# Kernel tuning notes

Measured on AMD Instinct MI355X. Metric: run time of the kernel, lower is better.

The kernel has to match this reference:

```python
import jax, jax.numpy as jnp
import numpy as np
from jax.scipy.special import logsumexp

N, C, D = 400000, 256, 3


def setup_inputs() -> dict:
    key = jax.random.key(0)
    k1, k2 = jax.random.split(key)
    X = jax.random.normal(k1, (N, D), dtype=jnp.float32)
    mu = jax.random.normal(k2, (C, D), dtype=jnp.float32)
    w = jnp.zeros((C,), dtype=jnp.float32)
    # sigma as in __init__: 0.1 * (r / C**(1/D)), r = sqrt(sum of per-dim variances of mu)
    r = jnp.sqrt(jnp.var(mu, axis=0).sum())
    sigma = (0.1 * (r / C ** (1.0 / D)))[None].astype(jnp.float32)
    return {"X": X, "mu": mu, "w": w, "sigma": sigma}


def reference(X, mu, w, sigma):
    """One EM step of the uniform-covariance GMM (no outliers). Returns (Y, Cfe)."""
    n, d = X.shape
    sig = sigma[0]
    # E-step: squared distances (N,C) and log-responsibilities
    D2_nc = jnp.sum((X[:, None, :] - mu[None, :, :]) ** 2, axis=-1)  # (N,C)
    loggaussnorm = d * (jnp.log(sig) + 0.5 * jnp.log(2.0 * jnp.pi))
    Zw = logsumexp(w)
    t_nc = w[None, :] - Zw - D2_nc / (2.0 * sig ** 2) - loggaussnorm  # (N,C)
    T_n = logsumexp(t_nc, axis=1)
    lgamma_nc = t_nc - T_n[:, None]
    gamma_nc = jnp.exp(lgamma_nc)
    # M-step updates (order matters, as in the torch code)
    mu_new = jax.nn.softmax(lgamma_nc, axis=0).T @ X            # (C,D)
    w_new = logsumexp(lgamma_nc, axis=0)                        # (C,)
    sig_new = jnp.sqrt(jnp.sum(gamma_nc * D2_nc) / (d * n))     # scalar
    # Quadratic targets Y_n = sum_c gamma_nc * mu_c (with updated mu)
    Y = gamma_nc @ mu_new                                       # (N,D)
    # Free-energy offset (loggaussnorm uses OLD sigma; 1/(2 sigma^2) uses NEW sigma)
    lpi_c = w_new - logsumexp(w_new)
    Cfe = jnp.sum(
        gamma_nc
        * (
            (jnp.sum(mu_new ** 2, axis=-1)[None, :] - jnp.sum(Y ** 2, axis=-1)[:, None])
            / (2.0 * sig_new ** 2)
            + loggaussnorm
            + lgamma_nc
            - lpi_c[None, :]
        )
    )
    return Y, Cfe
```

## Files before the change

kernel.cpp:

```cpp
#include <hip/hip_runtime.h>
#include <math.h>

#define CC   256
#define TILE 256

#define OFF_P     0
#define OFF_Q     1024
#define OFF_S     2048
#define OFF_CD    3072
#define OFF_CF    3080
#define OFF_T2    3088

__device__ __forceinline__ float fexp2(float x) { return __builtin_amdgcn_exp2f(x); }
__device__ __forceinline__ float flog2(float x) { return __builtin_amdgcn_logf(x); }

__global__ __launch_bounds__(256) void gmm_prep(const float* __restrict__ mu,
                                                const float* __restrict__ w,
                                                const float* __restrict__ sigma,
                                                float* __restrict__ ws)
{
    __shared__ float redA[4], redB[4];
    const int c = threadIdx.x;
    const int lane = c & 63, wid = c >> 6;

    ws[OFF_S + c] = 0.f; ws[OFF_S + 256 + c] = 0.f;
    ws[OFF_S + 512 + c] = 0.f; ws[OFF_S + 768 + c] = 0.f;
    if (c < 4) ((double*)(ws + OFF_CD))[c] = 0.0;
    if (c >= 8 && c < 16) ws[OFF_CF + (c - 6)] = 0.f;

    float wc = w[c];
    float m = wc;
    #pragma unroll
    for (int off = 32; off > 0; off >>= 1) m = fmaxf(m, __shfl_xor(m, off));
    if (lane == 0) redA[wid] = m;
    __syncthreads();
    m = fmaxf(fmaxf(redA[0], redA[1]), fmaxf(redA[2], redA[3]));
    float e = expf(wc - m);
    #pragma unroll
    for (int off = 32; off > 0; off >>= 1) e += __shfl_xor(e, off);
    if (lane == 0) redB[wid] = e;
    __syncthreads();
    float Zw = m + logf(redB[0] + redB[1] + redB[2] + redB[3]);

    const float L = 1.4426950408889634f;
    float sig = sigma[0];
    float lgn = 3.0f * (logf(sig) + 0.91893853320467274f);
    float k = L / (2.0f * sig * sig);
    float twok = 2.0f * k;
    float mx = mu[3*c], my = mu[3*c+1], mz = mu[3*c+2];
    float m2 = mx*mx + my*my + mz*mz;
    float alpha = (wc - Zw - lgn) * L - k * m2;
    ((float4*)(ws + OFF_P))[c] = make_float4(twok*mx, twok*my, twok*mz, alpha);
    if (c == 0) { ws[OFF_CF + 0] = twok; ws[OFF_CF + 1] = lgn; }
}

__global__ __launch_bounds__(256) void gmm_pass1(const float* __restrict__ X,
                                                 float* __restrict__ ws, int N)
{
    __shared__ float4 Psh[CC];
    __shared__ float4 XT[TILE];
    __shared__ float2 msP[2][TILE];
    __shared__ float4 Bpart[CC];
    __shared__ double redd[2][4];

    const int tid  = threadIdx.x;
    const int pi   = tid & 127;
    const int half = tid >> 7;
    const int n0   = blockIdx.x * TILE;
    const int NT   = min(TILE, N - n0);

    Psh[tid] = ((const float4*)(ws + OFF_P))[tid];

    const int i0 = pi, i1 = pi + 128;
    const bool v0 = i0 < NT, v1 = i1 < NT;
    float x0=0.f,y0=0.f,z0=0.f, x1=0.f,y1=0.f,z1=0.f;
    if (v0) { const float* p = X + 3*(size_t)(n0+i0); x0=p[0]; y0=p[1]; z0=p[2]; }
    if (v1) { const float* p = X + 3*(size_t)(n0+i1); x1=p[0]; y1=p[1]; z1=p[2]; }
    float q0 = fmaf(x0,x0, fmaf(y0,y0, z0*z0));
    float q1 = fmaf(x1,x1, fmaf(y1,y1, z1*z1));
    __syncthreads();

    const float4* Pc = Psh + half*128;
    float m0=-3.0e38f, m1=-3.0e38f, s0=0.f, s1=0.f;
    #pragma unroll 8
    for (int c = 0; c < 128; ++c) {
        float4 p = Pc[c];
        float u0 = fmaf(x0,p.x, fmaf(y0,p.y, fmaf(z0,p.z, p.w)));
        float u1 = fmaf(x1,p.x, fmaf(y1,p.y, fmaf(z1,p.z, p.w)));
        float a0 = fmaxf(m0,u0), a1 = fmaxf(m1,u1);
        if (__any((u0>m0) || (u1>m1))) {
            s0 *= fexp2(m0-a0); s1 *= fexp2(m1-a1);
            m0 = a0; m1 = a1;
        }
        s0 += fexp2(u0-m0);
        s1 += fexp2(u1-m1);
    }
    msP[half][i0] = make_float2(m0, s0);
    msP[half][i1] = make_float2(m1, s1);
    __syncthreads();

    double xd = 0.0, td = 0.0;
    if (half == 0) {
        if (v0) {
            float2 a = msP[0][i0], b = msP[1][i0];
            float M = fmaxf(a.x, b.x);
            float T2 = M + flog2(a.y*fexp2(a.x-M) + b.y*fexp2(b.x-M));
            XT[i0] = make_float4(x0,y0,z0,T2);
            ws[OFF_T2 + n0 + i0] = T2;
            xd += (double)q0; td += (double)T2;
        }
        if (v1) {
            float2 a = msP[0][i1], b = msP[1][i1];
            float M = fmaxf(a.x, b.x);
            float T2 = M + flog2(a.y*fexp2(a.x-M) + b.y*fexp2(b.x-M));
            XT[i1] = make_float4(x1,y1,z1,T2);
            ws[OFF_T2 + n0 + i1] = T2;
            xd += (double)q1; td += (double)T2;
        }
    }
    {
        const int lane = tid & 63, wid = tid >> 6;
        #pragma unroll
        for (int off = 32; off > 0; off >>= 1) { xd += __shfl_xor(xd, off); td += __shfl_xor(td, off); }
        if (lane == 0) { redd[0][wid] = xd; redd[1][wid] = td; }
    }
    __syncthreads();
    if (tid == 0) {
        double* CD = (double*)(ws + OFF_CD);
        atomicAdd(CD + 0, redd[0][0]+redd[0][1]+redd[0][2]+redd[0][3]);
        atomicAdd(CD + 1, redd[1][0]+redd[1][1]+redd[1][2]+redd[1][3]);
    }

    float4 pA = Psh[pi], pB = Psh[pi + 128];
    float SA=0.f,AxA=0.f,AyA=0.f,AzA=0.f, SB=0.f,AxB=0.f,AyB=0.f,AzB=0.f;
    const int nlo = half*128, nhi = min(nlo+128, NT);
    #pragma unroll 8
    for (int n = nlo; n < nhi; ++n) {
        float4 xt = XT[n];
        float uA = fmaf(xt.x,pA.x, fmaf(xt.y,pA.y, fmaf(xt.z,pA.z, pA.w)));
        float uB = fmaf(xt.x,pB.x, fmaf(xt.y,pB.y, fmaf(xt.z,pB.z, pB.w)));
        float gA = fexp2(uA - xt.w);
        float gB = fexp2(uB - xt.w);
        SA+=gA; AxA=fmaf(gA,xt.x,AxA); AyA=fmaf(gA,xt.y,AyA); AzA=fmaf(gA,xt.z,AzA);
        SB+=gB; AxB=fmaf(gB,xt.x,AxB); AyB=fmaf(gB,xt.y,AyB); AzB=fmaf(gB,xt.z,AzB);
    }
    if (half == 1) {
        Bpart[pi]       = make_float4(SA,AxA,AyA,AzA);
        Bpart[pi + 128] = make_float4(SB,AxB,AyB,AzB);
    }
    __syncthreads();
    if (half == 0) {
        float4 bA = Bpart[pi], bB = Bpart[pi + 128];
        SA+=bA.x; AxA+=bA.y; AyA+=bA.z; AzA+=bA.w;
        SB+=bB.x; AxB+=bB.y; AyB+=bB.z; AzB+=bB.w;
        float* Sg = ws + OFF_S;
        atomicAdd(Sg       + pi, SA);   atomicAdd(Sg       + pi + 128, SB);
        atomicAdd(Sg + 256 + pi, AxA);  atomicAdd(Sg + 256 + pi + 128, AxB);
        atomicAdd(Sg + 512 + pi, AyA);  atomicAdd(Sg + 512 + pi + 128, AyB);
        atomicAdd(Sg + 768 + pi, AzA);  atomicAdd(Sg + 768 + pi + 128, AzB);
    }
}

__global__ __launch_bounds__(256) void gmm_pass2(float* __restrict__ ws, int N)
{
    __shared__ double red6[6][4];
    const int c = threadIdx.x;
    const int lane = c & 63, wid = c >> 6;
    const float twok = ws[OFF_CF + 0];
    const double invt = 1.0 / (double)twok;
    double* CD = (double*)(ws + OFF_CD);

    float Sc  = ws[OFF_S       + c];
    float Axc = ws[OFF_S + 256 + c];
    float Ayc = ws[OFF_S + 512 + c];
    float Azc = ws[OFF_S + 768 + c];
    float4 p  = ((const float4*)(ws + OFF_P))[c];

    float inv = 1.0f / fmaxf(Sc, 1e-37f);
    float mx = Axc * inv, my = Ayc * inv, mz = Azc * inv;
    ((float4*)(ws + OFF_Q))[c] = make_float4(mx, my, mz, 0.f);

    double v0 = (double)Sc;
    double v1 = (double)Sc * (double)(mx*mx + my*my + mz*mz);
    double v2 = (double)Sc * log((double)fmaxf(Sc, 1e-37f));
    double v3 = (double)Sc * (double)(p.x*p.x + p.y*p.y + p.z*p.z);
    double v4 = (double)Sc * (double)p.w;
    double v5 = (double)(p.x*Axc + p.y*Ayc + p.z*Azc);

    #pragma unroll
    for (int off = 32; off > 0; off >>= 1) {
        v0 += __shfl_xor(v0, off); v1 += __shfl_xor(v1, off); v2 += __shfl_xor(v2, off);
        v3 += __shfl_xor(v3, off); v4 += __shfl_xor(v4, off); v5 += __shfl_xor(v5, off);
    }
    if (lane == 0) { red6[0][wid]=v0; red6[1][wid]=v1; red6[2][wid]=v2;
                     red6[3][wid]=v3; red6[4][wid]=v4; red6[5][wid]=v5; }
    __syncthreads();
    if (c == 0) {
        double sumS   = red6[0][0]+red6[0][1]+red6[0][2]+red6[0][3];
        double sumSM2 = red6[1][0]+red6[1][1]+red6[1][2]+red6[1][3];
        double sumSlS = red6[2][0]+red6[2][1]+red6[2][2]+red6[2][3];
        double sumMSs = red6[3][0]+red6[3][1]+red6[3][2]+red6[3][3];
        double sumAS  = red6[4][0]+red6[4][1]+red6[4][2]+red6[4][3];
        double dotMAs = red6[5][0]+red6[5][1]+red6[5][2]+red6[5][3];
        double sumX2  = CD[0];
        double sumT2  = CD[1];
        double sumGD2 = sumX2 + sumMSs*invt*invt - 2.0 * dotMAs*invt;
        double sn2    = sumGD2 / (3.0 * (double)N);
        ws[OFF_CF + 2] = (float)(1.0 / (2.0 * sn2));
        ws[OFF_CF + 3] = (float)(sumSlS - sumS * log(sumS));
        ws[OFF_CF + 4] = (float)(sumAS + dotMAs - sumT2);
        CD[3] = sumSM2;
    }
}

__global__ __launch_bounds__(256) void gmm_pass3(const float* __restrict__ X,
                                                 float* __restrict__ ws,
                                                 float* __restrict__ out, int N)
{
    __shared__ float4 Psh[CC], Qsh[CC];
    __shared__ float4 Yp[2][TILE];
    __shared__ double redd[4];

    const int tid  = threadIdx.x;
    const int pi   = tid & 127;
    const int half = tid >> 7;
    const int n0   = blockIdx.x * TILE;
    const int NT   = min(TILE, N - n0);

    Psh[tid] = ((const float4*)(ws + OFF_P))[tid];
    Qsh[tid] = ((const float4*)(ws + OFF_Q))[tid];

    const int i0 = pi, i1 = pi + 128;
    const bool v0 = i0 < NT, v1 = i1 < NT;
    float x0=0.f,y0=0.f,z0=0.f,T0=0.f, x1=0.f,y1=0.f,z1=0.f,T1=0.f;
    if (v0) { const float* p = X + 3*(size_t)(n0+i0); x0=p[0]; y0=p[1]; z0=p[2]; T0 = ws[OFF_T2+n0+i0]; }
    if (v1) { const float* p = X + 3*(size_t)(n0+i1); x1=p[0]; y1=p[1]; z1=p[2]; T1 = ws[OFF_T2+n0+i1]; }
    __syncthreads();

    const float4* Pc = Psh + half*128;
    const float4* Qc = Qsh + half*128;
    float Yx0=0.f,Yy0=0.f,Yz0=0.f, Yx1=0.f,Yy1=0.f,Yz1=0.f;
    #pragma unroll 8
    for (int c = 0; c < 128; ++c) {
        float4 p = Pc[c];
        float u0 = fmaf(x0,p.x, fmaf(y0,p.y, fmaf(z0,p.z, p.w)));
        float u1 = fmaf(x1,p.x, fmaf(y1,p.y, fmaf(z1,p.z, p.w)));
        float g0 = fexp2(u0 - T0);
        float g1 = fexp2(u1 - T1);
        float4 q = Qc[c];
        Yx0 = fmaf(g0,q.x,Yx0); Yy0 = fmaf(g0,q.y,Yy0); Yz0 = fmaf(g0,q.z,Yz0);
        Yx1 = fmaf(g1,q.x,Yx1); Yy1 = fmaf(g1,q.y,Yy1); Yz1 = fmaf(g1,q.z,Yz1);
    }
    Yp[half][i0] = make_float4(Yx0,Yy0,Yz0,0.f);
    Yp[half][i1] = make_float4(Yx1,Yy1,Yz1,0.f);
    __syncthreads();

    double y2d = 0.0;
    if (half == 0) {
        if (v0) {
            float4 a = Yp[0][i0], b = Yp[1][i0];
            float yx = a.x+b.x, yy = a.y+b.y, yz = a.z+b.z;
            float* op = out + 3*(size_t)(n0+i0);
            op[0]=yx; op[1]=yy; op[2]=yz;
            y2d += (double)yx*yx + (double)yy*yy + (double)yz*yz;
        }
        if (v1) {
            float4 a = Yp[0][i1], b = Yp[1][i1];
            float yx = a.x+b.x, yy = a.y+b.y, yz = a.z+b.z;
            float* op = out + 3*(size_t)(n0+i1);
            op[0]=yx; op[1]=yy; op[2]=yz;
            y2d += (double)yx*yx + (double)yy*yy + (double)yz*yz;
        }
    }
    {
        const int lane = tid & 63, wid = tid >> 6;
        #pragma unroll
        for (int off = 32; off > 0; off >>= 1) y2d += __shfl_xor(y2d, off);
        if (lane == 0) redd[wid] = y2d;
    }
    __syncthreads();
    if (tid == 0) atomicAdd(((double*)(ws + OFF_CD)) + 2, redd[0]+redd[1]+redd[2]+redd[3]);
}

__global__ void gmm_pass4(float* __restrict__ ws, float* __restrict__ cfe_out, int N)
{
    if (threadIdx.x == 0) {
        double* CD = (double*)(ws + OFF_CD);
        double Cfe = (CD[3] - CD[2]) * (double)ws[OFF_CF + 2]
                   + (double)N * (double)ws[OFF_CF + 1]
                   + 0.69314718055994531 * (double)ws[OFF_CF + 4]
                   - (double)ws[OFF_CF + 3];
        cfe_out[0] = (float)Cfe;
    }
}

extern "C" void kernel_launch(void* const* d_in, const int* in_sizes, int n_in,
                              void* d_out, int out_size, void* d_ws, size_t ws_size,
                              hipStream_t stream)
{
    const float* X     = (const float*)d_in[0];
    const float* mu    = (const float*)d_in[1];
    const float* w     = (const float*)d_in[2];
    const float* sigma = (const float*)d_in[3];
    float* out = (float*)d_out;
    float* ws  = (float*)d_ws;
    const int N = in_sizes[0] / 3;
    const int nblk = (N + TILE - 1) / TILE;

    gmm_prep <<<1,    256, 0, stream>>>(mu, w, sigma, ws);
    gmm_pass1<<<nblk, 256, 0, stream>>>(X, ws, N);
    gmm_pass2<<<1,    256, 0, stream>>>(ws, N);
    gmm_pass3<<<nblk, 256, 0, stream>>>(X, ws, out, N);
    gmm_pass4<<<1,    64,  0, stream>>>(ws, out + (size_t)3 * N, N);
}
```

Baseline: 112.6 us.

## Halve point tile to one point per thread and batch online-max rescaling

Shrinks the tile from 256 to 128 points so each thread handles one point instead of two in pass1 and pass3, doubling the grid and setting occupancy hints in launch bounds. The pass1 online logsumexp now computes 8 logits, takes their max, and does one wave-uniform rescale check per group instead of per component. This aims to raise occupancy and cut divergent branch overhead. The cost is that P/Q loads into shared memory and the atomics are amortized over fewer points, and the per-point work per loaded P entry is halved.

```diff
diff --git a/kernel.cpp b/kernel.cpp
--- a/kernel.cpp
+++ b/kernel.cpp
@@ -2,7 +2,7 @@
 #include <math.h>
 
 #define CC   256
-#define TILE 256
+#define TILE 128
 
 #define OFF_P     0
 #define OFF_Q     1024
@@ -54,8 +54,8 @@
     if (c == 0) { ws[OFF_CF + 0] = twok; ws[OFF_CF + 1] = lgn; }
 }
 
-__global__ __launch_bounds__(256) void gmm_pass1(const float* __restrict__ X,
-                                                 float* __restrict__ ws, int N)
+__global__ __launch_bounds__(256, 4) void gmm_pass1(const float* __restrict__ X,
+                                                    float* __restrict__ ws, int N)
 {
     __shared__ float4 Psh[CC];
     __shared__ float4 XT[TILE];
@@ -71,52 +71,43 @@
 
     Psh[tid] = ((const float4*)(ws + OFF_P))[tid];
 
-    const int i0 = pi, i1 = pi + 128;
-    const bool v0 = i0 < NT, v1 = i1 < NT;
-    float x0=0.f,y0=0.f,z0=0.f, x1=0.f,y1=0.f,z1=0.f;
-    if (v0) { const float* p = X + 3*(size_t)(n0+i0); x0=p[0]; y0=p[1]; z0=p[2]; }
-    if (v1) { const float* p = X + 3*(size_t)(n0+i1); x1=p[0]; y1=p[1]; z1=p[2]; }
+    const bool v0 = pi < NT;
+    float x0=0.f, y0=0.f, z0=0.f;
+    if (v0) { const float* p = X + 3*(size_t)(n0+pi); x0=p[0]; y0=p[1]; z0=p[2]; }
     float q0 = fmaf(x0,x0, fmaf(y0,y0, z0*z0));
-    float q1 = fmaf(x1,x1, fmaf(y1,y1, z1*z1));
     __syncthreads();
 
     const float4* Pc = Psh + half*128;
-    float m0=-3.0e38f, m1=-3.0e38f, s0=0.f, s1=0.f;
-    #pragma unroll 8
-    for (int c = 0; c < 128; ++c) {
-        float4 p = Pc[c];
-        float u0 = fmaf(x0,p.x, fmaf(y0,p.y, fmaf(z0,p.z, p.w)));
-        float u1 = fmaf(x1,p.x, fmaf(y1,p.y, fmaf(z1,p.z, p.w)));
-        float a0 = fmaxf(m0,u0), a1 = fmaxf(m1,u1);
-        if (__any((u0>m0) || (u1>m1))) {
-            s0 *= fexp2(m0-a0); s1 *= fexp2(m1-a1);
-            m0 = a0; m1 = a1;
+    float m0 = -3.0e38f, s0 = 0.f;
+    for (int c0 = 0; c0 < 128; c0 += 8) {
+        float u0[8];
+        #pragma unroll
+        for (int j = 0; j < 8; ++j) {
+            float4 p = Pc[c0 + j];
+            u0[j] = fmaf(x0,p.x, fmaf(y0,p.y, fmaf(z0,p.z, p.w)));
         }
-        s0 += fexp2(u0-m0);
-        s1 += fexp2(u1-m1);
-    }
-    msP[half][i0] = make_float2(m0, s0);
-    msP[half][i1] = make_float2(m1, s1);
+        float a = fmaxf(fmaxf(u0[0],u0[1]), fmaxf(u0[2],u0[3]));
+        float b = fmaxf(fmaxf(u0[4],u0[5]), fmaxf(u0[6],u0[7]));
+        float M = fmaxf(a, b);
+        if (__any(M > m0)) {
+            M = fmaxf(M, m0);
+            s0 *= fexp2(m0 - M);
+            m0 = M;
+        }
+        #pragma unroll
+        for (int j = 0; j < 8; ++j) s0 += fexp2(u0[j] - m0);
+    }
+    msP[half][pi] = make_float2(m0, s0);
     __syncthreads();
 
     double xd = 0.0, td = 0.0;
-    if (half == 0) {
-        if (v0) {
-            float2 a = msP[0][i0], b = msP[1][i0];
-            float M = fmaxf(a.x, b.x);
-            float T2 = M + flog2(a.y*fexp2(a.x-M) + b.y*fexp2(b.x-M));
-            XT[i0] = make_float4(x0,y0,z0,T2);
-            ws[OFF_T2 + n0 + i0] = T2;
-            xd += (double)q0; td += (double)T2;
-        }
-        if (v1) {
-            float2 a = msP[0][i1], b = msP[1][i1];
-            float M = fmaxf(a.x, b.x);
-            float T2 = M + flog2(a.y*fexp2(a.x-M) + b.y*fexp2(b.x-M));
-            XT[i1] = make_float4(x1,y1,z1,T2);
-            ws[OFF_T2 + n0 + i1] = T2;
-            xd += (double)q1; td += (double)T2;
-        }
+    if (half == 0 && v0) {
+        float2 a = msP[0][pi], b = msP[1][pi];
+        float M = fmaxf(a.x, b.x);
+        float T2 = M + flog2(a.y*fexp2(a.x-M) + b.y*fexp2(b.x-M));
+        XT[pi] = make_float4(x0,y0,z0,T2);
+        ws[OFF_T2 + n0 + pi] = T2;
+        xd = (double)q0; td = (double)T2;
     }
     {
         const int lane = tid & 63, wid = tid >> 6;
@@ -133,7 +124,7 @@
 
     float4 pA = Psh[pi], pB = Psh[pi + 128];
     float SA=0.f,AxA=0.f,AyA=0.f,AzA=0.f, SB=0.f,AxB=0.f,AyB=0.f,AzB=0.f;
-    const int nlo = half*128, nhi = min(nlo+128, NT);
+    const int nlo = half*64, nhi = min(nlo + 64, NT);
     #pragma unroll 8
     for (int n = nlo; n < nhi; ++n) {
         float4 xt = XT[n];
@@ -213,9 +204,9 @@
     }
 }
 
-__global__ __launch_bounds__(256) void gmm_pass3(const float* __restrict__ X,
-                                                 float* __restrict__ ws,
-                                                 float* __restrict__ out, int N)
+__global__ __launch_bounds__(256, 4) void gmm_pass3(const float* __restrict__ X,
+                                                    float* __restrict__ ws,
+                                                    float* __restrict__ out, int N)
 {
     __shared__ float4 Psh[CC], Qsh[CC];
     __shared__ float4 Yp[2][TILE];
@@ -230,47 +221,32 @@
     Psh[tid] = ((const float4*)(ws + OFF_P))[tid];
     Qsh[tid] = ((const float4*)(ws + OFF_Q))[tid];
 
-    const int i0 = pi, i1 = pi + 128;
-    const bool v0 = i0 < NT, v1 = i1 < NT;
-    float x0=0.f,y0=0.f,z0=0.f,T0=0.f, x1=0.f,y1=0.f,z1=0.f,T1=0.f;
-    if (v0) { const float* p = X + 3*(size_t)(n0+i0); x0=p[0]; y0=p[1]; z0=p[2]; T0 = ws[OFF_T2+n0+i0]; }
-    if (v1) { const float* p = X + 3*(size_t)(n0+i1); x1=p[0]; y1=p[1]; z1=p[2]; T1 = ws[OFF_T2+n0+i1]; }
+    const bool v0 = pi < NT;
+    float x0=0.f,y0=0.f,z0=0.f,T0=0.f;
+    if (v0) { const float* p = X + 3*(size_t)(n0+pi); x0=p[0]; y0=p[1]; z0=p[2]; T0 = ws[OFF_T2+n0+pi]; }
     __syncthreads();
 
     const float4* Pc = Psh + half*128;
     const float4* Qc = Qsh + half*128;
-    float Yx0=0.f,Yy0=0.f,Yz0=0.f, Yx1=0.f,Yy1=0.f,Yz1=0.f;
+    float Yx=0.f, Yy=0.f, Yz=0.f;
     #pragma unroll 8
     for (int c = 0; c < 128; ++c) {
         float4 p = Pc[c];
-        float u0 = fmaf(x0,p.x, fmaf(y0,p.y, fmaf(z0,p.z, p.w)));
-        float u1 = fmaf(x1,p.x, fmaf(y1,p.y, fmaf(z1,p.z, p.w)));
-        float g0 = fexp2(u0 - T0);
-        float g1 = fexp2(u1 - T1);
+        float u = fmaf(x0,p.x, fmaf(y0,p.y, fmaf(z0,p.z, p.w)));
+        float g = fexp2(u - T0);
         float4 q = Qc[c];
-        Yx0 = fmaf(g0,q.x,Yx0); Yy0 = fmaf(g0,q.y,Yy0); Yz0 = fmaf(g0,q.z,Yz0);
-        Yx1 = fmaf(g1,q.x,Yx1); Yy1 = fmaf(g1,q.y,Yy1); Yz1 = fmaf(g1,q.z,Yz1);
-    }
-    Yp[half][i0] = make_float4(Yx0,Yy0,Yz0,0.f);
-    Yp[half][i1] = make_float4(Yx1,Yy1,Yz1,0.f);
+        Yx = fmaf(g,q.x,Yx); Yy = fmaf(g,q.y,Yy); Yz = fmaf(g,q.z,Yz);
+    }
+    Yp[half][pi] = make_float4(Yx, Yy, Yz, 0.f);
     __syncthreads();
 
     double y2d = 0.0;
-    if (half == 0) {
-        if (v0) {
-            float4 a = Yp[0][i0], b = Yp[1][i0];
-            float yx = a.x+b.x, yy = a.y+b.y, yz = a.z+b.z;
-            float* op = out + 3*(size_t)(n0+i0);
-            op[0]=yx; op[1]=yy; op[2]=yz;
-            y2d += (double)yx*yx + (double)yy*yy + (double)yz*yz;
-        }
-        if (v1) {
-            float4 a = Yp[0][i1], b = Yp[1][i1];
-            float yx = a.x+b.x, yy = a.y+b.y, yz = a.z+b.z;
-            float* op = out + 3*(size_t)(n0+i1);
-            op[0]=yx; op[1]=yy; op[2]=yz;
-            y2d += (double)yx*yx + (double)yy*yy + (double)yz*yz;
-        }
+    if (half == 0 && v0) {
+        float4 a = Yp[0][pi], b = Yp[1][pi];
+        float yx = a.x+b.x, yy = a.y+b.y, yz = a.z+b.z;
+        float* op = out + 3*(size_t)(n0+pi);
+        op[0]=yx; op[1]=yy; op[2]=yz;
+        y2d = (double)yx*yx + (double)yy*yy + (double)yz*yz;
     }
     {
         const int lane = tid & 63, wid = tid >> 6;
```

Result: slower. 158.5 us (+40.7%).
